# Kernel optimization log

Hardware: AMD Instinct MI355X
Metric: run time of the kernel (lower is better)

## Reference

```python
import jax, jax.numpy as jnp
import numpy as np

N_NODES = 110
C = 4096  # in_channels = hidden = out_channels


def setup_inputs() -> dict:
    key = jax.random.key(0)
    ks = jax.random.split(key, 8)
    x = jax.random.normal(ks[0], (N_NODES, C), dtype=jnp.float32)
    adj = jax.random.randint(ks[1], (N_NODES, N_NODES), 0, 2, dtype=jnp.int32)
    # torch.nn.Linear weights stored [out_features, in_features]
    W2 = jax.random.normal(ks[2], (C, C), dtype=jnp.float32) / np.sqrt(C)
    b2 = jax.random.normal(ks[3], (C,), dtype=jnp.float32) * 0.01
    W1 = jax.random.normal(ks[4], (2 * C, C), dtype=jnp.float32) / np.sqrt(2 * C)
    b1 = jax.random.normal(ks[5], (C,), dtype=jnp.float32) * 0.01
    Wl = jax.random.normal(ks[6], (N_NODES, N_NODES), dtype=jnp.float32) / np.sqrt(N_NODES)
    bl = jax.random.normal(ks[7], (N_NODES,), dtype=jnp.float32) * 0.01
    # note: W1 is stored [in=2C, out=C]; W2 [in=C, out=C]; Wl [in=110, out=110]
    return {"x": x, "adj": adj, "W2": W2, "b2": b2, "W1": W1, "b1": b1, "Wl": Wl, "bl": bl}


def reference(x, adj, W2, b2, W1, b1, Wl, bl):
    # FeatGraphConv: h = lin2(x)
    h = x @ W2 + b2  # [N, C]
    # edge_index.nonzero(): adjacency -> edge list (i=src, j=dst); mean-aggregate
    # h[src] at dst. Dense equivalent: column-normalized mask matmul.
    mask = (adj != 0).astype(x.dtype)  # [N, N]
    deg = mask.sum(axis=0)  # in-degree of each target node j
    aggr = (mask.T @ h) / jnp.maximum(deg, 1.0)[:, None]  # [N, C]; 0 for isolated nodes (PyG mean)
    # update: lin1(cat(h, aggr)) then relu (in RegGNN.forward)
    out = jax.nn.relu(jnp.concatenate([h, aggr], axis=1) @ W1 + b1)  # [N, C]
    # x.t(); lin(110,110); x.t()
    out = (out.T @ Wl.T + bl).T  # [N, C]
    return out
```

## Files before the change

kernel.cpp:

```cpp
#include <hip/hip_runtime.h>
#include <hip/hip_fp16.h>

#define C 4096
#define NN 110
#define MPAD 112
#define NMT 7
#define KBS (NMT * 512)
#define NSLICE 8

typedef _Float16 f16x8 __attribute__((ext_vector_type(8)));
typedef float fx4 __attribute__((ext_vector_type(4)));
typedef unsigned long long ull;


__global__ __launch_bounds__(256)
void prep1_kernel(const float* __restrict__ x, _Float16* __restrict__ A1t,
                  const int* __restrict__ adj, ull* __restrict__ mlo,
                  ull* __restrict__ mhi, float* __restrict__ degs) {
    if (blockIdx.x == 224) {
        int j = threadIdx.x;
        if (j < NN) {
            ull lo = 0, hi = 0; int dg = 0;
            for (int i = 0; i < 64; ++i) {
                int m = (adj[i * NN + j] != 0);
                lo |= ((ull)m) << i; dg += m;
            }
            for (int i = 64; i < NN; ++i) {
                int m = (adj[i * NN + j] != 0);
                hi |= ((ull)m) << (i - 64); dg += m;
            }
            mlo[j] = lo; mhi[j] = hi;
            degs[j] = (float)(dg > 0 ? dg : 1);
        }
        return;
    }
    int u = blockIdx.x * 256 + threadIdx.x;
    int kb  = u / 448;
    int rem = u - kb * 448;
    int mt  = rem >> 6;
    int L   = rem & 63;
    int n   = mt * 16 + (L & 15);
    int c   = kb * 32 + (L >> 4) * 8;
    f16x8 hv;
    if (n < NN) {
        float4 v0 = *(const float4*)(x + (size_t)n * C + c);
        float4 v1 = *(const float4*)(x + (size_t)n * C + c + 4);
        hv[0]=(_Float16)v0.x; hv[1]=(_Float16)v0.y; hv[2]=(_Float16)v0.z; hv[3]=(_Float16)v0.w;
        hv[4]=(_Float16)v1.x; hv[5]=(_Float16)v1.y; hv[6]=(_Float16)v1.z; hv[7]=(_Float16)v1.w;
    } else {
        for (int e = 0; e < 8; ++e) hv[e] = (_Float16)0.f;
    }
    *(f16x8*)(A1t + (size_t)u * 8) = hv;
}

#define PIPE_BARRIER()                                                \
    do {                                                              \
        asm volatile("s_waitcnt lgkmcnt(0)" ::: "memory");            \
        __builtin_amdgcn_s_barrier();                                 \
        __builtin_amdgcn_sched_barrier(0);                            \
    } while (0)

template<int NITER>
__global__ __launch_bounds__(256, 2)
void mm_kernel(const _Float16* __restrict__ A, const float* __restrict__ B,
               float* __restrict__ Cpart) {
    __shared__ __align__(16) _Float16 Bs[2][64 * 64];

    const int t   = threadIdx.x;
    const int j0  = blockIdx.x * 64;
    const int w   = t >> 6;
    const int L   = t & 63;
    const int l15 = L & 15;
    const int q   = L >> 4;
    const int sc2 = (t & 31) * 2;
    const int kgr = (t >> 5) & 7;

    fx4 acc[7];
#pragma unroll
    for (int mt = 0; mt < 7; ++mt) acc[mt] = (fx4){0.f, 0.f, 0.f, 0.f};

    const float*    Bp  = B + (size_t)blockIdx.y * (NITER * 64) * C + j0 + sc2;
    const _Float16* ApL = A + (size_t)blockIdx.y * (NITER * 2) * KBS + L * 8;
    const _Float16* BsR = &Bs[0][0] + (w * 16 + l15) * 64;

    f16x8  af[2][2][7];
    float2 bva[8], bvb[8];

#define LOADAF(buf, ch)                                                        \
    { _Pragma("unroll")                                                        \
      for (int s = 0; s < 2; ++s)                                              \
          _Pragma("unroll")                                                    \
          for (int mt = 0; mt < 7; ++mt)                                       \
              af[buf][s][mt] = *(const f16x8*)(ApL                             \
                  + (size_t)((ch) * 2 + s) * KBS + mt * 512); }

#define LOADB(dst, ch)                                                         \
    { _Pragma("unroll")                                                        \
      for (int p = 0; p < 8; ++p)                                              \
          dst[p] = *(const float2*)(Bp + (size_t)((ch) * 64 + kgr * 8 + p) * C); }

#define COMMITB(src, buf)                                                      \
    { f16x8 h0, h1;                                                            \
      _Pragma("unroll")                                                        \
      for (int e = 0; e < 8; ++e) { h0[e] = (_Float16)src[e].x;                \
                                    h1[e] = (_Float16)src[e].y; }              \
      *(f16x8*)(&Bs[buf][0] + sc2 * 64 + ((kgr ^ (sc2 & 7)) << 3)) = h0;       \
      *(f16x8*)(&Bs[buf][0] + (sc2 + 1) * 64 + ((kgr ^ ((sc2 + 1) & 7)) << 3)) = h1; }

    LOADAF(0, 0);
    LOADB(bva, 0);
    COMMITB(bva, 0);
    LOADB(bva, 1);
    PIPE_BARRIER();

#pragma unroll
    for (int it = 0; it < NITER; ++it) {
        if (it + 1 < NITER) LOADAF((it + 1) & 1, it + 1);
        __builtin_amdgcn_sched_barrier(0);
        if (it + 2 < NITER) {
            if (it & 1) { LOADB(bva, it + 2); } else { LOADB(bvb, it + 2); }
        }
        __builtin_amdgcn_sched_barrier(0);
#pragma unroll
        for (int s = 0; s < 2; ++s) {
            f16x8 bf = *(const f16x8*)(BsR + (it & 1) * 4096
                            + ((((s << 2) + q) ^ (l15 & 7)) << 3));
#pragma unroll
            for (int mt = 0; mt < 7; ++mt)
                acc[mt] = __builtin_amdgcn_mfma_f32_16x16x32_f16(
                    af[it & 1][s][mt], bf, acc[mt], 0, 0, 0);
        }
        if (it + 1 < NITER) {
            if (it & 1) { COMMITB(bvb, (it + 1) & 1); }
            else        { COMMITB(bva, (it + 1) & 1); }
            PIPE_BARRIER();
        }
    }

    float* Cp = Cpart + (size_t)blockIdx.y * (NN * C) + j0 + w * 16 + l15;
#pragma unroll
    for (int mt = 0; mt < 7; ++mt)
#pragma unroll
        for (int r = 0; r < 4; ++r) {
            int row = mt * 16 + q * 4 + r;
            if (row < NN)
                Cp[(size_t)row * C] = acc[mt][r];
        }
#undef LOADAF
#undef LOADB
#undef COMMITB
}

__device__ __forceinline__ size_t fragidx(int n, int c) {
    return (size_t)(c >> 5) * KBS + (n >> 4) * 512
         + (((c >> 3) & 3) * 16 + (n & 15)) * 8 + (c & 7);
}

__global__ __launch_bounds__(256)
void agg_kernel(const float* __restrict__ hpart, const ull* __restrict__ gmlo,
                const ull* __restrict__ gmhi, const float* __restrict__ gdegs,
                const float* __restrict__ b2, _Float16* __restrict__ A3t) {
    __shared__ float hb[NN * 16];
    const int t  = threadIdx.x;
    const int c0 = blockIdx.x * 16;

    for (int idx = t; idx < NN * 8; idx += 256) {
        int n = idx >> 3, cp = (idx & 7) << 1;
        float v0 = b2[c0 + cp], v1 = b2[c0 + cp + 1];
#pragma unroll
        for (int p = 0; p < NSLICE; ++p) {
            float2 v = *(const float2*)(hpart + (size_t)p * (NN * C)
                                        + (size_t)n * C + c0 + cp);
            v0 += v.x; v1 += v.y;
        }
        hb[n * 16 + cp]     = v0;
        hb[n * 16 + cp + 1] = v1;
        union { _Float16 h[2]; unsigned u; } pk;
        pk.h[0] = (_Float16)v0;
        pk.h[1] = (_Float16)v1;
        *(unsigned*)(A3t + fragidx(n, c0 + cp)) = pk.u;
    }
    if (t < 32) {
        int n  = 110 + ((t >> 3) & 1);
        int hs = t >> 4;
        int cp = (t & 7) << 1;
        *(unsigned*)(A3t + fragidx(n, hs * C + c0 + cp)) = 0u;
    }
    __syncthreads();
    for (int idx = t; idx < NN * 8; idx += 256) {
        int j = idx >> 3, cp = (idx & 7) << 1;
        ull lo = gmlo[j], hi = gmhi[j];
        float dg = gdegs[j];
        float a0 = 0.f, a1 = 0.f;
        for (int i = 0; i < 64; ++i)
            if ((lo >> i) & 1) { a0 += hb[i * 16 + cp]; a1 += hb[i * 16 + cp + 1]; }
        for (int i = 64; i < NN; ++i)
            if ((hi >> (i - 64)) & 1) { a0 += hb[i * 16 + cp]; a1 += hb[i * 16 + cp + 1]; }
        union { _Float16 h[2]; unsigned u; } pk;
        pk.h[0] = (_Float16)(a0 / dg);
        pk.h[1] = (_Float16)(a1 / dg);
        *(unsigned*)(A3t + fragidx(j, C + c0 + cp)) = pk.u;
    }
}

__global__ __launch_bounds__(256)
void zred_kernel(const float* __restrict__ zpart, float* __restrict__ z_raw) {
    int idx = blockIdx.x * 256 + threadIdx.x;
    if (idx < NN * (C / 4)) {
        fx4 s = (fx4){0.f, 0.f, 0.f, 0.f};
#pragma unroll
        for (int p = 0; p < NSLICE; ++p) {
            fx4 v = *(const fx4*)(zpart + (size_t)p * (NN * C) + (size_t)idx * 4);
            s.x += v.x; s.y += v.y; s.z += v.z; s.w += v.w;
        }
        *(fx4*)(z_raw + (size_t)idx * 4) = s;
    }
}

__global__ __launch_bounds__(256)
void fin_kernel(const float* __restrict__ z_raw, const float* __restrict__ b1,
                const float* __restrict__ Wl, const float* __restrict__ bl,
                float* __restrict__ out) {
    __shared__ float zs[NN * 64];
    const int t  = threadIdx.x;
    const int c0 = blockIdx.x * 64;
    const int c  = t & 63;

    for (int idx = t; idx < NN * 64; idx += 256) {
        int k = idx >> 6, cc = idx & 63;
        float v = z_raw[(size_t)k * C + c0 + cc] + b1[c0 + cc];
        zs[idx] = fmaxf(v, 0.f);
    }
    __syncthreads();
    for (int jj = 0; jj < 7; ++jj) {
        int j = blockIdx.y * 28 + jj * 4 + (t >> 6);
        if (j < NN) {
            float a = bl[j];
#pragma unroll 2
            for (int k = 0; k < NN; ++k)
                a += Wl[j * NN + k] * zs[k * 64 + c];
            out[(size_t)j * C + c0 + c] = a;
        }
    }
}

extern "C" void kernel_launch(void* const* d_in, const int* in_sizes, int n_in,
                              void* d_out, int out_size, void* d_ws, size_t ws_size,
                              hipStream_t stream) {
    const float* x   = (const float*)d_in[0];
    const int*   adj = (const int*)d_in[1];
    const float* W2  = (const float*)d_in[2];
    const float* b2  = (const float*)d_in[3];
    const float* W1  = (const float*)d_in[4];
    const float* b1  = (const float*)d_in[5];
    const float* Wl  = (const float*)d_in[6];
    const float* bl  = (const float*)d_in[7];
    float* out = (float*)d_out;

    char* ws = (char*)d_ws;
    float*    hpart = (float*)(ws);
    float*    zpart = (float*)(ws + 14417920);
    float*    z_raw = (float*)(ws + 28835840);
    _Float16* A1t   = (_Float16*)(ws + 30638080);
    _Float16* A3t   = (_Float16*)(ws + 31555584);
    ull*      mlo   = (ull*)(ws + 33390592);
    ull*      mhi   = (ull*)(ws + 33391472);
    float*    degs  = (float*)(ws + 33392352);

    prep1_kernel<<<225, 256, 0, stream>>>(x, A1t, adj, mlo, mhi, degs);
    mm_kernel<8><<<dim3(64, NSLICE), 256, 0, stream>>>(A1t, W2, hpart);
    agg_kernel<<<C / 16, 256, 0, stream>>>(hpart, mlo, mhi, degs, b2, A3t);
    mm_kernel<16><<<dim3(64, NSLICE), 256, 0, stream>>>(A3t, W1, zpart);
    zred_kernel<<<440, 256, 0, stream>>>(zpart, z_raw);
    fin_kernel<<<dim3(C / 64, 4), 256, 0, stream>>>(z_raw, b1, Wl, bl, out);
}
```

Measured before the change: 347.8 us.

## Load B weights directly into registers, dropping LDS staging and barriers

The matmul kernel no longer stages the fp32 weight tile through shared memory with swizzled fp16 commits and block barriers. Each lane now loads its own B column elements straight from global memory as scalar strided loads, converts them to fp16 in registers, and feeds them to MFMA. This removes the LDS writes and reads and the per-iteration barriers, but replaces coalesced float2 loads with scalar loads strided by C. Every wave fetches its own column slice, so memory coalescing and load-instruction count may get worse.

Result: slower. 361.5 us (+3.9%).

```diff
diff --git a/kernel.cpp b/kernel.cpp
--- a/kernel.cpp
+++ b/kernel.cpp
@@ -3,7 +3,6 @@
 
 #define C 4096
 #define NN 110
-#define MPAD 112
 #define NMT 7
 #define KBS (NMT * 512)
 #define NSLICE 8
@@ -12,6 +11,10 @@
 typedef float fx4 __attribute__((ext_vector_type(4)));
 typedef unsigned long long ull;
 
+__device__ __forceinline__ size_t fragidx(int n, int c) {
+    return (size_t)(c >> 5) * KBS + (n >> 4) * 512
+         + (((c >> 3) & 3) * 16 + (n & 15)) * 8 + (c & 7);
+}
 
 __global__ __launch_bounds__(256)
 void prep1_kernel(const float* __restrict__ x, _Float16* __restrict__ A1t,
@@ -53,38 +56,28 @@
     *(f16x8*)(A1t + (size_t)u * 8) = hv;
 }
 
-#define PIPE_BARRIER()                                                \
-    do {                                                              \
-        asm volatile("s_waitcnt lgkmcnt(0)" ::: "memory");            \
-        __builtin_amdgcn_s_barrier();                                 \
-        __builtin_amdgcn_sched_barrier(0);                            \
-    } while (0)
-
 template<int NITER>
 __global__ __launch_bounds__(256, 2)
 void mm_kernel(const _Float16* __restrict__ A, const float* __restrict__ B,
                float* __restrict__ Cpart) {
-    __shared__ __align__(16) _Float16 Bs[2][64 * 64];
-
     const int t   = threadIdx.x;
     const int j0  = blockIdx.x * 64;
+    const int y   = blockIdx.y;
     const int w   = t >> 6;
     const int L   = t & 63;
     const int l15 = L & 15;
     const int q   = L >> 4;
-    const int sc2 = (t & 31) * 2;
-    const int kgr = (t >> 5) & 7;
+    const int qq8 = q * 8;
 
     fx4 acc[7];
 #pragma unroll
     for (int mt = 0; mt < 7; ++mt) acc[mt] = (fx4){0.f, 0.f, 0.f, 0.f};
 
-    const float*    Bp  = B + (size_t)blockIdx.y * (NITER * 64) * C + j0 + sc2;
-    const _Float16* ApL = A + (size_t)blockIdx.y * (NITER * 2) * KBS + L * 8;
-    const _Float16* BsR = &Bs[0][0] + (w * 16 + l15) * 64;
-
-    f16x8  af[2][2][7];
-    float2 bva[8], bvb[8];
+    const _Float16* ApL  = A + (size_t)y * (NITER * 2) * KBS + L * 8;
+    const float*    Bcol = B + (size_t)y * (NITER * 64) * C + j0 + w * 16 + l15;
+
+    f16x8 af[2][2][7];
+    float bw[2][2][8];
 
 #define LOADAF(buf, ch)                                                        \
     { _Pragma("unroll")                                                        \
@@ -94,50 +87,36 @@
               af[buf][s][mt] = *(const f16x8*)(ApL                             \
                   + (size_t)((ch) * 2 + s) * KBS + mt * 512); }
 
-#define LOADB(dst, ch)                                                         \
+#define LOADBW(buf, ch)                                                        \
     { _Pragma("unroll")                                                        \
-      for (int p = 0; p < 8; ++p)                                              \
-          dst[p] = *(const float2*)(Bp + (size_t)((ch) * 64 + kgr * 8 + p) * C); }
-
-#define COMMITB(src, buf)                                                      \
-    { f16x8 h0, h1;                                                            \
-      _Pragma("unroll")                                                        \
-      for (int e = 0; e < 8; ++e) { h0[e] = (_Float16)src[e].x;                \
-                                    h1[e] = (_Float16)src[e].y; }              \
-      *(f16x8*)(&Bs[buf][0] + sc2 * 64 + ((kgr ^ (sc2 & 7)) << 3)) = h0;       \
-      *(f16x8*)(&Bs[buf][0] + (sc2 + 1) * 64 + ((kgr ^ ((sc2 + 1) & 7)) << 3)) = h1; }
+      for (int s = 0; s < 2; ++s)                                              \
+          _Pragma("unroll")                                                    \
+          for (int e = 0; e < 8; ++e)                                          \
+              bw[buf][s][e] =                                                  \
+                  Bcol[(size_t)((ch) * 64 + s * 32 + qq8 + e) * C]; }
 
     LOADAF(0, 0);
-    LOADB(bva, 0);
-    COMMITB(bva, 0);
-    LOADB(bva, 1);
-    PIPE_BARRIER();
+    LOADBW(0, 0);
 
 #pragma unroll
     for (int it = 0; it < NITER; ++it) {
-        if (it + 1 < NITER) LOADAF((it + 1) & 1, it + 1);
-        __builtin_amdgcn_sched_barrier(0);
-        if (it + 2 < NITER) {
-            if (it & 1) { LOADB(bva, it + 2); } else { LOADB(bvb, it + 2); }
-        }
-        __builtin_amdgcn_sched_barrier(0);
+        if (it + 1 < NITER) {
+            LOADAF((it + 1) & 1, it + 1);
+            LOADBW((it + 1) & 1, it + 1);
+        }
 #pragma unroll
         for (int s = 0; s < 2; ++s) {
-            f16x8 bf = *(const f16x8*)(BsR + (it & 1) * 4096
-                            + ((((s << 2) + q) ^ (l15 & 7)) << 3));
+            f16x8 bf;
+#pragma unroll
+            for (int e = 0; e < 8; ++e) bf[e] = (_Float16)bw[it & 1][s][e];
 #pragma unroll
             for (int mt = 0; mt < 7; ++mt)
                 acc[mt] = __builtin_amdgcn_mfma_f32_16x16x32_f16(
                     af[it & 1][s][mt], bf, acc[mt], 0, 0, 0);
         }
-        if (it + 1 < NITER) {
-            if (it & 1) { COMMITB(bvb, (it + 1) & 1); }
-            else        { COMMITB(bva, (it + 1) & 1); }
-            PIPE_BARRIER();
-        }
-    }
-
-    float* Cp = Cpart + (size_t)blockIdx.y * (NN * C) + j0 + w * 16 + l15;
+    }
+
+    float* Cp = Cpart + (size_t)y * (NN * C) + j0 + w * 16 + l15;
 #pragma unroll
     for (int mt = 0; mt < 7; ++mt)
 #pragma unroll
@@ -147,13 +126,7 @@
                 Cp[(size_t)row * C] = acc[mt][r];
         }
 #undef LOADAF
-#undef LOADB
-#undef COMMITB
-}
-
-__device__ __forceinline__ size_t fragidx(int n, int c) {
-    return (size_t)(c >> 5) * KBS + (n >> 4) * 512
-         + (((c >> 3) & 3) * 16 + (n & 15)) * 8 + (c & 7);
+#undef LOADBW
 }
 
 __global__ __launch_bounds__(256)
```
